# Kernel tuning notes

Hardware: AMD Instinct MI355X
Metric: run time of the kernel (lower is better)

## Reference

```python
import jax, jax.numpy as jnp
import numpy as np


def setup_inputs() -> dict:
    key = jax.random.key(0)
    ks = jax.random.split(key, 7)
    B, F, D = 1024, 32, 64
    H = [128, 128, 128]
    x = jax.random.normal(ks[0], (B, F, D), dtype=jnp.float32)
    # Conv1d(k=1) weights: (out, in) where in = prev_field * F, Kaiming-ish scale
    W0 = jax.random.normal(ks[1], (H[0], F * F), dtype=jnp.float32) * 0.02
    b0 = jnp.zeros((H[0],), dtype=jnp.float32)
    W1 = jax.random.normal(ks[2], (H[1], H[0] * F), dtype=jnp.float32) * 0.02
    b1 = jnp.zeros((H[1],), dtype=jnp.float32)
    W2 = jax.random.normal(ks[3], (H[2], H[1] * F), dtype=jnp.float32) * 0.02
    b2 = jnp.zeros((H[2],), dtype=jnp.float32)
    return {"x": x, "W0": W0, "b0": b0, "W1": W1, "b1": b1, "W2": W2, "b2": b2}


def reference(x, W0, b0, W1, b1, W2, b2):
    # CIN: per layer, outer product of current hidden with base fields along
    # embed dim, then 1x1 conv (channel mix) + ReLU. We fuse the bhmd
    # intermediate directly into the contraction: W reshaped to (o, h, m)
    # matches torch's reshape(b, h*m, d) channel ordering (h major, m minor).
    F = x.shape[1]
    x0 = x  # (b, m=F, d)
    h = x
    res = []
    for W, b in ((W0, b0), (W1, b1), (W2, b2)):
        o = W.shape[0]
        Wr = W.reshape(o, h.shape[1], F)  # (o, h, m)
        z = jnp.einsum('bhd,bmd,ohm->bod', h, x0, Wr) + b[None, :, None]
        h = jax.nn.relu(z)
        res.append(h)
    out = jnp.concatenate(res, axis=1)  # (b, sum(H), d)
    return jnp.sum(out, axis=-1)  # (b, sum(H))
```

## Files before the change

kernel.cpp:

```cpp
#include <hip/hip_runtime.h>
#include <stdint.h>


typedef __attribute__((ext_vector_type(8))) _Float16 f16x8;
typedef __attribute__((ext_vector_type(2))) _Float16 f16x2;
typedef __attribute__((ext_vector_type(4))) float f32x4;
typedef __attribute__((ext_vector_type(16))) float f32x16;
typedef __attribute__((ext_vector_type(4))) int i32x4;

union AB {
  i32x4 i;
  f16x8 h;
  uint32_t u[4];
};

static __device__ __forceinline__ uint32_t pkmul(uint32_t a, uint32_t b) {
  f16x2 r = __builtin_bit_cast(f16x2, a) * __builtin_bit_cast(f16x2, b);
  return __builtin_bit_cast(uint32_t, r);
}
static __device__ __forceinline__ uint32_t pkcvt(float a, float b) {
  return __builtin_bit_cast(uint32_t, __builtin_amdgcn_cvt_pkrtz(a, b));
}

#define HP 136

__global__ __launch_bounds__(256, 4) void cin_main(
    const float* __restrict__ x, const uint16_t* __restrict__ wp,
    const float* __restrict__ bias0, const float* __restrict__ bias1,
    const float* __restrict__ bias2, float* __restrict__ out) {
  __shared__ __align__(16) uint16_t hT[64][HP];

  const int tid = threadIdx.x;
  const int ot = tid >> 6, lane = tid & 63;
  const int hi = lane >> 5;
  const int l31 = lane & 31;
  const int b = blockIdx.x;

  for (int e = tid; e < 2048; e += 256) {
    int m = e >> 6, d = e & 63;
    hT[d][m] =
        __builtin_bit_cast(uint16_t, (_Float16)x[(size_t)b * 2048 + m * 64 + d]);
  }
  __syncthreads();

  AB xf[2][2];
#pragma unroll
  for (int dt = 0; dt < 2; ++dt)
#pragma unroll
    for (int s = 0; s < 2; ++s)
      xf[dt][s].i = *(const i32x4*)&hT[dt * 32 + l31][s * 16 + hi * 8];

  f32x16 acc0, acc1;

#pragma unroll
  for (int L = 0; L < 3; ++L) {
    const int Kch = (L == 0) ? 32 : 128;
    const uint16_t* wl = (L == 0) ? wp : (L == 1) ? wp + 131072 : wp + 655360;
    const float* bias = (L == 0) ? bias0 : (L == 1) ? bias1 : bias2;

    const uint16_t* wptr = wl + (size_t)ot * Kch * 1024 + lane * 8;

#pragma unroll
    for (int r = 0; r < 16; ++r) { acc0[r] = 0.f; acc1[r] = 0.f; }

    AB wbuf[2][4];
    uint32_t hvA[2], hvB[2];

    auto loadSlot = [&](int sl, int c) {
      int cw = (c < Kch) ? c : 0;
#pragma unroll
      for (int cc = 0; cc < 2; ++cc)
#pragma unroll
        for (int s = 0; s < 2; ++s)
          wbuf[sl][cc * 2 + s].i =
              *(const i32x4*)(wptr + (size_t)(cw + cc) * 1024 + s * 512);
    };
    auto loadHv = [&](uint32_t (&hv)[2], int c) {
      int cw = (c < Kch) ? c : 0;
#pragma unroll
      for (int dt = 0; dt < 2; ++dt)
        hv[dt] = *(const uint32_t*)&hT[dt * 32 + l31][cw];
    };
    auto computeStep = [&](const AB (&wb)[4], const uint32_t (&hv)[2]) {
#pragma unroll
      for (int cc = 0; cc < 2; ++cc) {
        uint32_t hd0 = __builtin_amdgcn_perm(hv[0], hv[0],
                                             cc ? 0x03020302u : 0x01000100u);
        uint32_t hd1 = __builtin_amdgcn_perm(hv[1], hv[1],
                                             cc ? 0x03020302u : 0x01000100u);
#pragma unroll
        for (int s = 0; s < 2; ++s) {
          AB bf0, bf1;
#pragma unroll
          for (int k = 0; k < 4; ++k) {
            bf0.u[k] = pkmul(hd0, xf[0][s].u[k]);
            bf1.u[k] = pkmul(hd1, xf[1][s].u[k]);
          }
          acc0 = __builtin_amdgcn_mfma_f32_32x32x16_f16(wb[cc * 2 + s].h,
                                                        bf0.h, acc0, 0, 0, 0);
          acc1 = __builtin_amdgcn_mfma_f32_32x32x16_f16(wb[cc * 2 + s].h,
                                                        bf1.h, acc1, 0, 0, 0);
        }
      }
    };

    loadSlot(0, 0);
    loadSlot(1, 2);
    loadHv(hvA, 0);

#pragma unroll 1
    for (int c0 = 0; c0 < Kch; c0 += 4) {
      loadHv(hvB, c0 + 2);
      computeStep(wbuf[0], hvA);
      loadSlot(0, c0 + 4);
      __builtin_amdgcn_sched_barrier(0);
      loadHv(hvA, c0 + 4);
      computeStep(wbuf[1], hvB);
      loadSlot(1, c0 + 6);
      __builtin_amdgcn_sched_barrier(0);
    }

    f32x4 bv[4];
#pragma unroll
    for (int rg = 0; rg < 4; ++rg)
      bv[rg] = *(const f32x4*)(bias + ot * 32 + 8 * rg + 4 * hi);
#pragma unroll
    for (int r = 0; r < 16; ++r) {
      acc0[r] = fmaxf(acc0[r] + bv[r >> 2][r & 3], 0.f);
      acc1[r] = fmaxf(acc1[r] + bv[r >> 2][r & 3], 0.f);
    }

    if (L < 2) {
      __syncthreads();
#pragma unroll
      for (int rg = 0; rg < 4; ++rg) {
        uint2 pk0, pk1;
        pk0.x = pkcvt(acc0[4 * rg + 0], acc0[4 * rg + 1]);
        pk0.y = pkcvt(acc0[4 * rg + 2], acc0[4 * rg + 3]);
        pk1.x = pkcvt(acc1[4 * rg + 0], acc1[4 * rg + 1]);
        pk1.y = pkcvt(acc1[4 * rg + 2], acc1[4 * rg + 3]);
        int ch = ot * 32 + 8 * rg + 4 * hi;
        *(uint2*)&hT[l31][ch] = pk0;
        *(uint2*)&hT[32 + l31][ch] = pk1;
      }
    }

#pragma unroll
    for (int rg = 0; rg < 4; ++rg) {
      f32x4 s4;
#pragma unroll
      for (int rr = 0; rr < 4; ++rr) {
        float s = acc0[4 * rg + rr] + acc1[4 * rg + rr];
        s += __shfl_xor(s, 1);
        s += __shfl_xor(s, 2);
        s += __shfl_xor(s, 4);
        s += __shfl_xor(s, 8);
        s += __shfl_xor(s, 16);
        s4[rr] = s;
      }
      if (l31 == 0)
        *(f32x4*)(out + (size_t)b * 384 + L * 128 + ot * 32 + 8 * rg + 4 * hi) = s4;
    }

    if (L < 2) __syncthreads();
  }
}

__global__ void pack_w_all(const float* __restrict__ W0, const float* __restrict__ W1,
                           const float* __restrict__ W2, uint16_t* __restrict__ Wp) {
  int blk = blockIdx.x;
  const float* W;
  uint16_t* dst;
  int kshift;
  if (blk < 64)       { W = W0; dst = Wp;          kshift = 5; }
  else if (blk < 320) { W = W1; dst = Wp + 131072; kshift = 7; blk -= 64; }
  else                { W = W2; dst = Wp + 655360; kshift = 7; blk -= 320; }
  int idx = blk * 256 + threadIdx.x;
  int Kq = 1 << (kshift + 2);
  int o = idx >> (kshift + 2);
  int kq = idx & (Kq - 1);
  int c = kq >> 2, s = (kq >> 1) & 1, hi = kq & 1;
  int ot = o >> 5, li = o & 31;
  const float* src = W + ((size_t)o << (kshift + 5)) + kq * 8;
  uint4 val;
  val.x = pkcvt(src[0], src[1]);
  val.y = pkcvt(src[2], src[3]);
  val.z = pkcvt(src[4], src[5]);
  val.w = pkcvt(src[6], src[7]);
  size_t d16 = ((((size_t)(ot << kshift) + c) * 2 + s) << 9) + (hi << 8) + (li << 3);
  *(uint4*)(dst + d16) = val;
}

extern "C" void kernel_launch(void* const* d_in, const int* in_sizes, int n_in,
                              void* d_out, int out_size, void* d_ws, size_t ws_size,
                              hipStream_t stream) {
  (void)in_sizes; (void)n_in; (void)out_size; (void)ws_size;
  const float* x  = (const float*)d_in[0];
  const float* W0 = (const float*)d_in[1];
  const float* b0 = (const float*)d_in[2];
  const float* W1 = (const float*)d_in[3];
  const float* b1 = (const float*)d_in[4];
  const float* W2 = (const float*)d_in[5];
  const float* b2 = (const float*)d_in[6];
  uint16_t* wpacked = (uint16_t*)d_ws;

  hipLaunchKernelGGL(pack_w_all, dim3(576), dim3(256), 0, stream, W0, W1, W2, wpacked);
  hipLaunchKernelGGL(cin_main, dim3(1024), dim3(256), 0, stream,
                     x, wpacked, b0, b1, b2, (float*)d_out);
}
```

Measured before the change: 214.8 us.

## Split warps over output-channel pairs and d-halves to reuse outer-product B fragments

Work is remapped so each wave owns two 32-channel output tiles for one 32-wide half of the embedding dimension, instead of one output tile for both halves. Each computed outer-product B fragment is now reused by two MFMAs, halving the pkmul work per MFMA, while each wave loads two weight streams. Partial sums across the two d-halves are combined through a shared-memory buffer, which adds a barrier. The last loop iteration is peeled to drop the out-of-range clamp on prefetches, the LDS pad changes to 140, and the launch bound drops to 3 blocks per CU to allow more registers.

```diff
diff --git a/kernel.cpp b/kernel.cpp
--- a/kernel.cpp
+++ b/kernel.cpp
@@ -7,12 +7,17 @@
 typedef __attribute__((ext_vector_type(4))) float f32x4;
 typedef __attribute__((ext_vector_type(16))) float f32x16;
 typedef __attribute__((ext_vector_type(4))) int i32x4;
+typedef __attribute__((ext_vector_type(2))) int i32x2;
 
 union AB {
   i32x4 i;
   f16x8 h;
   uint32_t u[4];
 };
+union AB2 {
+  i32x2 i;
+  uint32_t u[2];
+};
 
 static __device__ __forceinline__ uint32_t pkmul(uint32_t a, uint32_t b) {
   f16x2 r = __builtin_bit_cast(f16x2, a) * __builtin_bit_cast(f16x2, b);
@@ -22,18 +27,22 @@
   return __builtin_bit_cast(uint32_t, __builtin_amdgcn_cvt_pkrtz(a, b));
 }
 
-#define HP 136
-
-__global__ __launch_bounds__(256, 4) void cin_main(
+#define HP 140
+
+__global__ __launch_bounds__(256, 3) void cin_main(
     const float* __restrict__ x, const uint16_t* __restrict__ wp,
     const float* __restrict__ bias0, const float* __restrict__ bias1,
     const float* __restrict__ bias2, float* __restrict__ out) {
   __shared__ __align__(16) uint16_t hT[64][HP];
+  __shared__ float psum[2][128];
 
   const int tid = threadIdx.x;
-  const int ot = tid >> 6, lane = tid & 63;
+  const int w = tid >> 6, lane = tid & 63;
+  const int og = w & 1;
+  const int dt = w >> 1;
   const int hi = lane >> 5;
   const int l31 = lane & 31;
+  const int lane8 = lane * 8;
   const int b = blockIdx.x;
 
   for (int e = tid; e < 2048; e += 256) {
@@ -43,14 +52,20 @@
   }
   __syncthreads();
 
-  AB xf[2][2];
-#pragma unroll
-  for (int dt = 0; dt < 2; ++dt)
-#pragma unroll
-    for (int s = 0; s < 2; ++s)
-      xf[dt][s].i = *(const i32x4*)&hT[dt * 32 + l31][s * 16 + hi * 8];
-
-  f32x16 acc0, acc1;
+  const int drow = dt * 32 + l31;
+
+  AB xf[2];
+#pragma unroll
+  for (int s = 0; s < 2; ++s) {
+    AB2 lo = *(const AB2*)&hT[drow][s * 16 + hi * 8];
+    AB2 hi4 = *(const AB2*)&hT[drow][s * 16 + hi * 8 + 4];
+    xf[s].u[0] = lo.u[0];
+    xf[s].u[1] = lo.u[1];
+    xf[s].u[2] = hi4.u[0];
+    xf[s].u[3] = hi4.u[1];
+  }
+
+  f32x16 acc[2];
 
 #pragma unroll
   for (int L = 0; L < 3; ++L) {
@@ -58,48 +73,47 @@
     const uint16_t* wl = (L == 0) ? wp : (L == 1) ? wp + 131072 : wp + 655360;
     const float* bias = (L == 0) ? bias0 : (L == 1) ? bias1 : bias2;
 
-    const uint16_t* wptr = wl + (size_t)ot * Kch * 1024 + lane * 8;
-
-#pragma unroll
-    for (int r = 0; r < 16; ++r) { acc0[r] = 0.f; acc1[r] = 0.f; }
-
-    AB wbuf[2][4];
-    uint32_t hvA[2], hvB[2];
+    const uint16_t* pb0 =
+        wl + ((size_t)__builtin_amdgcn_readfirstlane((og * 2 + 0) * Kch) << 10);
+    const uint16_t* pb1 =
+        wl + ((size_t)__builtin_amdgcn_readfirstlane((og * 2 + 1) * Kch) << 10);
+
+#pragma unroll
+    for (int o2 = 0; o2 < 2; ++o2)
+#pragma unroll
+      for (int r = 0; r < 16; ++r) acc[o2][r] = 0.f;
+
+    AB wbuf[2][2][2][2];
+    uint32_t hvA, hvB;
 
     auto loadSlot = [&](int sl, int c) {
-      int cw = (c < Kch) ? c : 0;
 #pragma unroll
       for (int cc = 0; cc < 2; ++cc)
 #pragma unroll
-        for (int s = 0; s < 2; ++s)
-          wbuf[sl][cc * 2 + s].i =
-              *(const i32x4*)(wptr + (size_t)(cw + cc) * 1024 + s * 512);
+        for (int s = 0; s < 2; ++s) {
+          wbuf[sl][cc][s][0].i =
+              *(const i32x4*)(pb0 + ((c + cc) << 10) + (s << 9) + lane8);
+          wbuf[sl][cc][s][1].i =
+              *(const i32x4*)(pb1 + ((c + cc) << 10) + (s << 9) + lane8);
+        }
     };
-    auto loadHv = [&](uint32_t (&hv)[2], int c) {
-      int cw = (c < Kch) ? c : 0;
-#pragma unroll
-      for (int dt = 0; dt < 2; ++dt)
-        hv[dt] = *(const uint32_t*)&hT[dt * 32 + l31][cw];
+    auto loadHv = [&](uint32_t& hv, int c) {
+      hv = *(const uint32_t*)&hT[drow][c];
     };
-    auto computeStep = [&](const AB (&wb)[4], const uint32_t (&hv)[2]) {
+    auto compute2 = [&](const AB (&wb)[2][2][2], uint32_t hv) {
 #pragma unroll
       for (int cc = 0; cc < 2; ++cc) {
-        uint32_t hd0 = __builtin_amdgcn_perm(hv[0], hv[0],
-                                             cc ? 0x03020302u : 0x01000100u);
-        uint32_t hd1 = __builtin_amdgcn_perm(hv[1], hv[1],
-                                             cc ? 0x03020302u : 0x01000100u);
+        uint32_t hd = __builtin_amdgcn_perm(hv, hv,
+                                            cc ? 0x03020302u : 0x01000100u);
 #pragma unroll
         for (int s = 0; s < 2; ++s) {
-          AB bf0, bf1;
-#pragma unroll
-          for (int k = 0; k < 4; ++k) {
-            bf0.u[k] = pkmul(hd0, xf[0][s].u[k]);
-            bf1.u[k] = pkmul(hd1, xf[1][s].u[k]);
-          }
-          acc0 = __builtin_amdgcn_mfma_f32_32x32x16_f16(wb[cc * 2 + s].h,
-                                                        bf0.h, acc0, 0, 0, 0);
-          acc1 = __builtin_amdgcn_mfma_f32_32x32x16_f16(wb[cc * 2 + s].h,
-                                                        bf1.h, acc1, 0, 0, 0);
+          AB bf;
+#pragma unroll
+          for (int k = 0; k < 4; ++k) bf.u[k] = pkmul(hd, xf[s].u[k]);
+          acc[0] = __builtin_amdgcn_mfma_f32_32x32x16_f16(wb[cc][s][0].h, bf.h,
+                                                          acc[0], 0, 0, 0);
+          acc[1] = __builtin_amdgcn_mfma_f32_32x32x16_f16(wb[cc][s][1].h, bf.h,
+                                                          acc[1], 0, 0, 0);
         }
       }
     };
@@ -109,58 +123,61 @@
     loadHv(hvA, 0);
 
 #pragma unroll 1
-    for (int c0 = 0; c0 < Kch; c0 += 4) {
+    for (int c0 = 0; c0 < Kch - 4; c0 += 4) {
       loadHv(hvB, c0 + 2);
-      computeStep(wbuf[0], hvA);
+      compute2(wbuf[0], hvA);
       loadSlot(0, c0 + 4);
       __builtin_amdgcn_sched_barrier(0);
       loadHv(hvA, c0 + 4);
-      computeStep(wbuf[1], hvB);
+      compute2(wbuf[1], hvB);
       loadSlot(1, c0 + 6);
       __builtin_amdgcn_sched_barrier(0);
     }
-
-    f32x4 bv[4];
-#pragma unroll
-    for (int rg = 0; rg < 4; ++rg)
-      bv[rg] = *(const f32x4*)(bias + ot * 32 + 8 * rg + 4 * hi);
-#pragma unroll
-    for (int r = 0; r < 16; ++r) {
-      acc0[r] = fmaxf(acc0[r] + bv[r >> 2][r & 3], 0.f);
-      acc1[r] = fmaxf(acc1[r] + bv[r >> 2][r & 3], 0.f);
-    }
+    loadHv(hvB, Kch - 2);
+    compute2(wbuf[0], hvA);
+    compute2(wbuf[1], hvB);
+
+#pragma unroll
+    for (int o2 = 0; o2 < 2; ++o2)
+#pragma unroll
+      for (int rg = 0; rg < 4; ++rg) {
+        f32x4 bv = *(const f32x4*)(bias + og * 64 + o2 * 32 + 8 * rg + 4 * hi);
+#pragma unroll
+        for (int rr = 0; rr < 4; ++rr)
+          acc[o2][4 * rg + rr] = fmaxf(acc[o2][4 * rg + rr] + bv[rr], 0.f);
+      }
 
     if (L < 2) {
       __syncthreads();
 #pragma unroll
-      for (int rg = 0; rg < 4; ++rg) {
-        uint2 pk0, pk1;
-        pk0.x = pkcvt(acc0[4 * rg + 0], acc0[4 * rg + 1]);
-        pk0.y = pkcvt(acc0[4 * rg + 2], acc0[4 * rg + 3]);
-        pk1.x = pkcvt(acc1[4 * rg + 0], acc1[4 * rg + 1]);
-        pk1.y = pkcvt(acc1[4 * rg + 2], acc1[4 * rg + 3]);
-        int ch = ot * 32 + 8 * rg + 4 * hi;
-        *(uint2*)&hT[l31][ch] = pk0;
-        *(uint2*)&hT[32 + l31][ch] = pk1;
-      }
+      for (int o2 = 0; o2 < 2; ++o2)
+#pragma unroll
+        for (int rg = 0; rg < 4; ++rg) {
+          uint2 pk;
+          pk.x = pkcvt(acc[o2][4 * rg + 0], acc[o2][4 * rg + 1]);
+          pk.y = pkcvt(acc[o2][4 * rg + 2], acc[o2][4 * rg + 3]);
+          *(uint2*)&hT[drow][og * 64 + o2 * 32 + 8 * rg + 4 * hi] = pk;
+        }
     }
 
 #pragma unroll
-    for (int rg = 0; rg < 4; ++rg) {
-      f32x4 s4;
-#pragma unroll
-      for (int rr = 0; rr < 4; ++rr) {
-        float s = acc0[4 * rg + rr] + acc1[4 * rg + rr];
-        s += __shfl_xor(s, 1);
-        s += __shfl_xor(s, 2);
-        s += __shfl_xor(s, 4);
-        s += __shfl_xor(s, 8);
-        s += __shfl_xor(s, 16);
-        s4[rr] = s;
-      }
-      if (l31 == 0)
-        *(f32x4*)(out + (size_t)b * 384 + L * 128 + ot * 32 + 8 * rg + 4 * hi) = s4;
-    }
+    for (int o2 = 0; o2 < 2; ++o2)
+#pragma unroll
+      for (int rg = 0; rg < 4; ++rg)
+#pragma unroll
+        for (int rr = 0; rr < 4; ++rr) {
+          float s = acc[o2][4 * rg + rr];
+          s += __shfl_xor(s, 1);
+          s += __shfl_xor(s, 2);
+          s += __shfl_xor(s, 4);
+          s += __shfl_xor(s, 8);
+          s += __shfl_xor(s, 16);
+          if (l31 == 0)
+            psum[dt][og * 64 + o2 * 32 + 8 * rg + 4 * hi + rr] = s;
+        }
+    __syncthreads();
+    if (tid < 128)
+      out[(size_t)b * 384 + L * 128 + tid] = psum[0][tid] + psum[1][tid];
 
     if (L < 2) __syncthreads();
   }
```

Result: slower. 252.9 us (+17.8%).
